# Kernel tuning notes

Hardware: AMD Instinct MI355X
Metric: run time of the kernel (lower is better)

## Reference

```python
import jax, jax.numpy as jnp
import numpy as np
from jax import lax

BATCH, FS, DIM = 32, 7, 512
E, TOPK, KD = 4, 2, 4            # experts, top-k, scan directions
N_STATE, DT_RANK = 16, 32
CAP_FACTOR, EPS, AUX_W = 1.25, 1e-6, 0.01


def _layernorm(x, g, b, eps=1e-5):
    mu = x.mean(-1, keepdims=True)
    var = ((x - mu) ** 2).mean(-1, keepdims=True)
    return (x - mu) * lax.rsqrt(var + eps) * g + b


def setup_inputs() -> dict:
    key = jax.random.key(0)
    ks = jax.random.split(key, 10)
    s = 0.02
    d = DIM
    return {
        "x": jax.random.normal(ks[0], (BATCH, FS, FS, d), jnp.float32),
        "w_gate": jax.random.normal(ks[1], (d, E)) * s,
        "b_gate": jnp.zeros((E,), jnp.float32),
        "in_proj_w": jax.random.normal(ks[2], (E, d, 2 * d)) * s,
        "in_proj_b": jnp.zeros((E, 2 * d), jnp.float32),
        "conv_w": jax.random.normal(ks[3], (E, d, 3, 3)) * s,
        "conv_b": jnp.zeros((E, d), jnp.float32),
        "x_proj_w": jax.random.normal(ks[4], (E, KD, DT_RANK + 2 * N_STATE, d)) * s,
        "dt_proj_w": jax.random.normal(ks[5], (E, KD, d, DT_RANK)) * s,
        "dt_proj_b": jax.random.normal(ks[6], (E, KD, d)) * 0.1,
        "A_log": jnp.log(jax.random.uniform(ks[7], (E, KD, d, N_STATE), minval=1.0, maxval=16.0)),
        "Ds": jnp.ones((E, KD, d), jnp.float32),
        "out_norm_g": jnp.ones((E, d), jnp.float32),
        "out_norm_b": jnp.zeros((E, d), jnp.float32),
        "norm_g": jnp.ones((E, d), jnp.float32),
        "norm_b": jnp.zeros((E, d), jnp.float32),
    }


def _ss2d_expert(x, in_w, in_b, cw, cb, xpw, dtw, dtb, A_log, Ds, og, ob, ng, nb):
    # x: [B,H,W,d]; one SS2D expert (VMamba-style, use_out_proj=False, out_norm=True)
    B, H, W, d = x.shape
    L = H * W
    xz = x @ in_w + in_b                      # [B,H,W,2d]
    xin, z = jnp.split(xz, 2, axis=-1)
    xc = jnp.transpose(xin, (0, 3, 1, 2))     # [B,d,H,W]
    xc = lax.conv_general_dilated(xc, cw[:, None, :, :], (1, 1), 'SAME',
                                  feature_group_count=d,
                                  dimension_numbers=('NCHW', 'OIHW', 'NCHW'))
    xc = jax.nn.silu(xc + cb[None, :, None, None])
    xh = xc.reshape(B, d, L)                              # row-major (h)
    xv = jnp.transpose(xc, (0, 1, 3, 2)).reshape(B, d, L)  # col-major (v)
    xs = jnp.stack([xh, xh[..., ::-1], xv, xv[..., ::-1]], axis=1)  # [B,K,d,L]

    x_dbl = jnp.einsum('bkdl,kcd->bkcl', xs, xpw)
    dt, Bm, Cm = jnp.split(x_dbl, [DT_RANK, DT_RANK + N_STATE], axis=2)
    dt = jnp.einsum('bkrl,kdr->bkdl', dt, dtw) + dtb[None, :, :, None]
    dt = jax.nn.softplus(dt)                  # [B,K,d,L]
    A = -jnp.exp(A_log)                       # [K,d,N]

    def step(h, inp):
        dt_t, B_t, C_t, x_t = inp             # [B,K,d],[B,K,N],[B,K,N],[B,K,d]
        h = h * jnp.exp(dt_t[..., None] * A) + (dt_t * x_t)[..., None] * B_t[:, :, None, :]
        y = jnp.einsum('bkdn,bkn->bkd', h, C_t)
        return h, y

    h0 = jnp.zeros((B, KD, d, N_STATE), x.dtype)
    seq = (jnp.moveaxis(dt, 3, 0), jnp.moveaxis(Bm, 3, 0),
           jnp.moveaxis(Cm, 3, 0), jnp.moveaxis(xs, 3, 0))
    _, ys = lax.scan(step, h0, seq)           # [L,B,K,d]
    ys = jnp.moveaxis(ys, 0, 3) + Ds[None, :, :, None] * xs  # [B,K,d,L]

    y = ys[:, 0] + ys[:, 1, :, ::-1]
    yv = ys[:, 2] + ys[:, 3, :, ::-1]
    y = y + jnp.transpose(yv.reshape(B, d, W, H), (0, 1, 3, 2)).reshape(B, d, L)
    y = jnp.transpose(y.reshape(B, d, H, W), (0, 2, 3, 1))   # [B,H,W,d]
    y = _layernorm(y, og, ob) * jax.nn.silu(z)
    pooled = y.mean(axis=(1, 2))              # adaptive avg pool -> [B,d]
    return _layernorm(pooled, ng, nb)


def reference(x, w_gate, b_gate, in_proj_w, in_proj_b, conv_w, conv_b, x_proj_w,
              dt_proj_w, dt_proj_b, A_log, Ds, out_norm_g, out_norm_b, norm_g, norm_b):
    B = x.shape[0]
    # gate on globally pooled features
    x_flat = x.mean(axis=(1, 2))                              # [B,dim]
    raw = jax.nn.softmax(x_flat @ w_gate + b_gate, axis=-1)   # [B,E]
    capacity = int(CAP_FACTOR * B)
    _, idx = lax.top_k(raw, TOPK)
    mask = jax.nn.one_hot(idx, E, dtype=raw.dtype).sum(axis=1)  # [B,E]
    masked = raw * mask
    denom = masked.sum(0, keepdims=True) + EPS
    gate_scores = masked / denom * capacity
    importance = raw.mean(0)
    load = mask.mean(0)
    aux_loss = AUX_W * jnp.mean((load - importance) ** 2)

    topv, topi = lax.top_k(gate_scores, TOPK)                 # [B,k]
    # dense dispatch: run every expert on the full batch (E small), then gather
    all_out = jax.vmap(_ss2d_expert, in_axes=(None,) + (0,) * 13)(
        x, in_proj_w, in_proj_b, conv_w, conv_b, x_proj_w, dt_proj_w, dt_proj_b,
        A_log, Ds, out_norm_g, out_norm_b, norm_g, norm_b)    # [E,B,dim]
    sel = all_out[topi, jnp.arange(B)[:, None]]               # [B,k,dim]
    mixed = (topv[..., None] * sel).sum(axis=1)               # [B,dim]
    return mixed, aux_loss
```

## Files before the change

### kernel.cpp

```cpp
#include <hip/hip_runtime.h>
#include <hip/hip_bf16.h>

#define B_   32
#define D_   512
#define L_   49
#define E_   4
#define KD_  4
#define NS_  16
#define RK_  32
#define JOBS_ 64

typedef short s16x8 __attribute__((ext_vector_type(8)));
typedef float f32x4v __attribute__((ext_vector_type(4)));
union U4 { uint4 u; s16x8 s; unsigned short us[8]; };

__device__ __forceinline__ float bf2f(unsigned short u){
  union{unsigned int i; float f;} v; v.i = ((unsigned int)u)<<16; return v.f;
}
__device__ __forceinline__ float2 bfp(unsigned int u){
  union{unsigned int i; float f;} a, b; a.i = u<<16; b.i = u & 0xffff0000u;
  return make_float2(a.f, b.f);
}
__device__ __forceinline__ unsigned short f2bfu(float f){
  union{float f; unsigned int i;} u; u.f = f;
  unsigned int r = u.i + 0x7fffu + ((u.i >> 16) & 1u);
  return (unsigned short)(r >> 16);
}
__device__ __forceinline__ float silu_f(float x){ return x / (1.f + expf(-x)); }

__device__ __forceinline__ float fast_exp2(float x){
  return __builtin_amdgcn_exp2f(x);
}
__device__ __forceinline__ float quad_add4(float y){
  float t1 = __uint_as_float(__builtin_amdgcn_mov_dpp(__float_as_uint(y), 0xB1, 0xF, 0xF, true));
  y += t1;
  float t2 = __uint_as_float(__builtin_amdgcn_mov_dpp(__float_as_uint(y), 0x4E, 0xF, 0xF, true));
  y += t2;
  return y;
}
__device__ __forceinline__ unsigned cvtpk_bf16(float lo, float hi){
  unsigned r; asm("v_cvt_pk_bf16_f32 %0, %1, %2" : "=v"(r) : "v"(lo), "v"(hi)); return r;
}

__device__ __forceinline__ int detect_bf(const void* x){
  unsigned short u = ((const unsigned short*)x)[threadIdx.x & 63];
  int e = (u >> 7) & 0xff;
  unsigned long long m = __ballot(e >= 96 && e < 160);
  return __popcll(m) >= 56;
}

__device__ __forceinline__ float ldf(const void* p, size_t i, int bf){
  return bf ? bf2f(((const unsigned short*)p)[i]) : ((const float*)p)[i];
}
struct f8s{ float v[8]; };
__device__ __forceinline__ f8s ldf8(const void* p, size_t i, int bf){
  f8s r;
  if (bf){
    uint4 u = *(const uint4*)((const unsigned short*)p + i);
    float2 x = bfp(u.x), y = bfp(u.y), z = bfp(u.z), w = bfp(u.w);
    r.v[0]=x.x; r.v[1]=x.y; r.v[2]=y.x; r.v[3]=y.y;
    r.v[4]=z.x; r.v[5]=z.y; r.v[6]=w.x; r.v[7]=w.y;
  } else {
    const float4* q = (const float4*)((const float*)p + i);
    float4 a = q[0], b = q[1];
    r.v[0]=a.x; r.v[1]=a.y; r.v[2]=a.z; r.v[3]=a.w;
    r.v[4]=b.x; r.v[5]=b.y; r.v[6]=b.z; r.v[7]=b.w;
  }
  return r;
}
struct f4s{ float v[4]; };
__device__ __forceinline__ f4s ldf4(const void* p, size_t i, int bf){
  f4s r;
  if (bf){
    uint2 u = *(const uint2*)((const unsigned short*)p + i);
    float2 a = bfp(u.x), b = bfp(u.y);
    r.v[0]=a.x; r.v[1]=a.y; r.v[2]=b.x; r.v[3]=b.y;
  } else {
    float4 a = *(const float4*)((const float*)p + i);
    r.v[0]=a.x; r.v[1]=a.y; r.v[2]=a.z; r.v[3]=a.w;
  }
  return r;
}
__device__ __forceinline__ U4 ldbf8(const void* p, size_t i, int bf){
  U4 r;
  if (bf){
    r.u = *(const uint4*)((const unsigned short*)p + i);
  } else {
    const float* q = (const float*)p + i;
    float4 a = *(const float4*)q, b = *(const float4*)(q+4);
    r.u.x = (unsigned)f2bfu(a.x) | ((unsigned)f2bfu(a.y) << 16);
    r.u.y = (unsigned)f2bfu(a.z) | ((unsigned)f2bfu(a.w) << 16);
    r.u.z = (unsigned)f2bfu(b.x) | ((unsigned)f2bfu(b.y) << 16);
    r.u.w = (unsigned)f2bfu(b.z) | ((unsigned)f2bfu(b.w) << 16);
  }
  return r;
}
__device__ __forceinline__ void split8(const float av[8], U4& hi, U4& lo){
  #pragma unroll
  for (int j = 0; j < 8; j++){
    union{float f; unsigned int i;} u; u.f = av[j];
    unsigned short h = (unsigned short)(u.i >> 16);
    hi.us[j] = h;
    lo.us[j] = f2bfu(av[j] - bf2f(h));
  }
}

__device__ __forceinline__ int dirmap(int k, int l){
  if (k == 0) return l;
  if (k == 1) return 48 - l;
  if (k == 2) return (l % 7) * 7 + l / 7;
  int l2 = 48 - l; return (l2 % 7) * 7 + l2 / 7;
}

__global__ __launch_bounds__(256) void k_prep(const void* __restrict__ x,
                                              const void* __restrict__ w,
                                              const void* __restrict__ wg,
                                              const void* __restrict__ bg,
                                              unsigned short* __restrict__ wt,
                                              unsigned short* __restrict__ xbf,
                                              float* __restrict__ logits){
  __shared__ unsigned short tile[64][72];
  __shared__ float red[4][4];
  __shared__ float pool[4][512];
  int bf = detect_bf(x);
  int blk = blockIdx.x;
  int t = threadIdx.x;
  if (blk < 512){
    int e = blk >> 7, cb = (blk >> 3) & 15, db = blk & 7;
    #pragma unroll
    for (int r = 0; r < 4; r++){
      int d  = r*16 + (t>>4);
      int c0 = (t&15)*4;
      size_t g = ((size_t)e*512 + db*64 + d)*1024 + cb*64 + c0;
      if (bf){
        uint2 u = *(const uint2*)((const unsigned short*)w + g);
        tile[c0+0][d] = (unsigned short)(u.x & 0xffffu);
        tile[c0+1][d] = (unsigned short)(u.x >> 16);
        tile[c0+2][d] = (unsigned short)(u.y & 0xffffu);
        tile[c0+3][d] = (unsigned short)(u.y >> 16);
      } else {
        float4 v = *(const float4*)((const float*)w + g);
        tile[c0+0][d] = f2bfu(v.x);
        tile[c0+1][d] = f2bfu(v.y);
        tile[c0+2][d] = f2bfu(v.z);
        tile[c0+3][d] = f2bfu(v.w);
      }
    }
    __syncthreads();
    #pragma unroll
    for (int r = 0; r < 2; r++){
      int o = r*256 + t;
      int c = o >> 3, d0 = (o & 7)*8;
      uint4 v = *(const uint4*)&tile[c][d0];
      *(uint4*)(wt + ((size_t)e*1024 + cb*64 + c)*512 + db*64 + d0) = v;
    }
  } else {
    int b = blk - 512;
    int wave = t >> 6, lane = t & 63;
    int d0 = lane * 8;
    float s8[8] = {};
    for (int l = wave; l < L_; l += 4){
      size_t ix = ((size_t)(b*L_ + l))*D_ + d0;
      U4 xb;
      if (bf){
        xb.u = *(const uint4*)((const unsigned short*)x + ix);
        float2 a = bfp(xb.u.x), bq = bfp(xb.u.y), c = bfp(xb.u.z), dq = bfp(xb.u.w);
        s8[0] += a.x;  s8[1] += a.y;  s8[2] += bq.x; s8[3] += bq.y;
        s8[4] += c.x;  s8[5] += c.y;  s8[6] += dq.x; s8[7] += dq.y;
      } else {
        const float* q = (const float*)x + ix;
        float4 f0 = *(const float4*)q, f1 = *(const float4*)(q+4);
        float av[8] = {f0.x,f0.y,f0.z,f0.w, f1.x,f1.y,f1.z,f1.w};
        #pragma unroll
        for (int j = 0; j < 8; j++){ xb.us[j] = f2bfu(av[j]); s8[j] += av[j]; }
      }
      *(uint4*)(xbf + ix) = xb.u;
    }
    #pragma unroll
    for (int j = 0; j < 8; j++) pool[wave][d0+j] = s8[j];
    __syncthreads();
    float p[4] = {0.f, 0.f, 0.f, 0.f};
    #pragma unroll
    for (int rep = 0; rep < 2; rep++){
      int d = t + rep*256;
      float s = pool[0][d] + pool[1][d] + pool[2][d] + pool[3][d];
      float xfd = s * (1.f/49.f);
      #pragma unroll
      for (int e = 0; e < 4; e++) p[e] = fmaf(xfd, ldf(wg, (size_t)d*E_ + e, bf), p[e]);
    }
    #pragma unroll
    for (int off = 32; off > 0; off >>= 1){
      #pragma unroll
      for (int e = 0; e < 4; e++) p[e] += __shfl_down(p[e], off, 64);
    }
    if (lane == 0){
      #pragma unroll
      for (int e = 0; e < 4; e++) red[wave][e] = p[e];
    }
    __syncthreads();
    if (t < 4)
      logits[b*4 + t] = red[0][t]+red[1][t]+red[2][t]+red[3][t] + ldf(bg, t, bf);
  }
}

__global__ __launch_bounds__(128) void k_gate2(const void* __restrict__ x,
                                               const float* __restrict__ logits,
                                               int* __restrict__ topi, float* __restrict__ topv,
                                               void* __restrict__ out){
  __shared__ float raw[B_*E_];
  __shared__ int   sel[B_];
  __shared__ float den[E_], auxp[E_];
  int bf = detect_bf(x);
  int t = threadIdx.x;
  if (t < B_){
    float l0=logits[t*4+0], l1=logits[t*4+1], l2=logits[t*4+2], l3=logits[t*4+3];
    float m = fmaxf(fmaxf(l0,l1), fmaxf(l2,l3));
    float e0=expf(l0-m), e1=expf(l1-m), e2=expf(l2-m), e3=expf(l3-m);
    float s = e0+e1+e2+e3;
    float r[4] = {e0/s, e1/s, e2/s, e3/s};
    int i1 = 0; float v1 = r[0];
    for (int e = 1; e < 4; e++) if (r[e] > v1){ v1 = r[e]; i1 = e; }
    int i2 = -1; float v2 = -1.f;
    for (int e = 0; e < 4; e++){ if (e == i1) continue; if (r[e] > v2){ v2 = r[e]; i2 = e; } }
    if (i1 < 0 || i1 > 3) i1 = 0;
    if (i2 < 0 || i2 > 3) i2 = (i1 + 1) & 3;
    sel[t] = (1<<i1) | (1<<i2);
    for (int e = 0; e < 4; e++) raw[t*4+e] = r[e];
  }
  __syncthreads();
  if (t < E_){
    float dn = 0.f, imp = 0.f, ld = 0.f;
    for (int b = 0; b < B_; b++){
      float r = raw[b*4+t];
      int bit = (sel[b] >> t) & 1;
      if (bit) dn += r;
      imp += r; ld += (float)bit;
    }
    den[t] = dn + 1e-6f;
    imp *= (1.f/B_); ld *= (1.f/B_);
    float df = ld - imp; auxp[t] = df*df;
  }
  __syncthreads();
  if (t == 0){
    float a = 0.01f * 0.25f * (auxp[0]+auxp[1]+auxp[2]+auxp[3]);
    if (bf) ((unsigned short*)out)[16384] = f2bfu(a);
    else    ((float*)out)[16384] = a;
  }
  if (t < B_){
    float gs[4];
    for (int e = 0; e < 4; e++){
      int bit = (sel[t] >> e) & 1;
      gs[e] = bit ? raw[t*4+e] * 40.f / den[e] : 0.f;
    }
    int i1 = 0; float v1 = gs[0];
    for (int e = 1; e < 4; e++) if (gs[e] > v1){ v1 = gs[e]; i1 = e; }
    int i2 = -1; float v2 = -1e30f;
    for (int e = 0; e < 4; e++){ if (e == i1) continue; if (gs[e] > v2){ v2 = gs[e]; i2 = e; } }
    if (i1 < 0 || i1 > 3) i1 = 0;
    if (i2 < 0 || i2 > 3) i2 = (i1 + 1) & 3;
    topi[t*2+0] = i1; topv[t*2+0] = v1;
    topi[t*2+1] = i2; topv[t*2+1] = v2;
  }
}

__global__ __launch_bounds__(256, 4) void k_inproj_mfma(const void* __restrict__ x,
                                                     const unsigned short* __restrict__ xbf,
                                                     const unsigned short* __restrict__ wt,
                                                     const void* __restrict__ bias,
                                                     const void* __restrict__ cw,
                                                     const void* __restrict__ cb,
                                                     const int* __restrict__ topi,
                                                     unsigned short* __restrict__ zbuf,
                                                     float* __restrict__ xc,
                                                     unsigned short* __restrict__ xchi,
                                                     unsigned short* __restrict__ xclo){
  __shared__ float xzt[49*68];
  int bf = detect_bf(x);
  int job = blockIdx.x, nt = blockIdx.y;
  int b = job >> 1;
  int e = topi[job];
  int t = threadIdx.x;
  int wave = t >> 6, lane = t & 63;
  int l16 = lane & 15, quad = lane >> 4;
  int arow = wave*16 + l16; if (arow > 48) arow = 48;
  size_t abase = ((size_t)(b*L_ + arow))*D_;
  int ct = nt*64;
  size_t bbase = ((size_t)(e*1024 + ct + l16))*D_;
  f32x4v acc[4] = {};
  for (int k0 = 0; k0 < 512; k0 += 32){
    int k = k0 + quad*8;
    U4 a; a.u = *(const uint4*)(xbf + abase + k);
    #pragma unroll
    for (int s = 0; s < 4; s++){
      U4 bb;
      bb.u = *(const uint4*)(wt + bbase + (size_t)s*16*D_ + k);
      acc[s] = __builtin_amdgcn_mfma_f32_16x16x32_bf16(a.s, bb.s, acc[s], 0, 0, 0);
    }
  }
  int rb = wave*16 + quad*4;
  if (nt >= 8){
    #pragma unroll
    for (int s = 0; s < 4; s++){
      int c = ct + s*16 + l16;
      float bv = ldf(bias, (size_t)e*1024 + c, bf);
      #pragma unroll
      for (int r = 0; r < 4; r++){
        int row = rb + r;
        if (row < L_)
          zbuf[(size_t)job*25088 + row*D_ + (c - 512)] = f2bfu(acc[s][r] + bv);
      }
    }
    return;
  }
  #pragma unroll
  for (int s = 0; s < 4; s++){
    int cl = s*16 + l16;
    float bv = ldf(bias, (size_t)e*1024 + ct + cl, bf);
    #pragma unroll
    for (int r = 0; r < 4; r++){
      int row = rb + r;
      if (row < L_) xzt[row*68 + cl] = acc[s][r] + bv;
    }
  }
  __syncthreads();
  int c = t & 63, pg = t >> 6;
  int dch = ct + c;
  float wv[9];
  #pragma unroll
  for (int j = 0; j < 9; j++) wv[j] = ldf(cw, ((size_t)(e*D_ + dch))*9 + j, bf);
  float cbv = ldf(cb, (size_t)e*D_ + dch, bf);
  for (int p = pg; p < L_; p += 4){
    int h = p / 7, w = p % 7;
    float a2 = cbv;
    #pragma unroll
    for (int dy = 0; dy < 3; dy++){
      int hh = h + dy - 1; if (hh < 0 || hh >= 7) continue;
      #pragma unroll
      for (int dx = 0; dx < 3; dx++){
        int ww = w + dx - 1; if (ww < 0 || ww >= 7) continue;
        a2 = fmaf(xzt[(hh*7+ww)*68 + c], wv[dy*3+dx], a2);
      }
    }
    float sv = a2 * (1.f/(1.f+expf(-a2)));
    size_t oix = (size_t)job*25088 + (size_t)p*D_ + dch;
    xc[oix] = sv;
    unsigned int ui = __float_as_uint(sv);
    unsigned short hh2 = (unsigned short)(ui >> 16);
    xchi[oix] = hh2;
    xclo[oix] = f2bfu(sv - bf2f(hh2));
  }
}

__global__ __launch_bounds__(256, 4) void k_xproj(const void* __restrict__ x,
                                               const void* __restrict__ xpw,
                                               const int* __restrict__ topi,
                                               const unsigned short* __restrict__ xchi,
                                               const unsigned short* __restrict__ xclo,
                                               float* __restrict__ xdbl){
  int bf = detect_bf(x);
  int kq = blockIdx.x, job = blockIdx.y;
  int k = kq & 3, q = kq >> 2;
  int t = threadIdx.x;
  int wave = t >> 6, lane = t & 63;
  int l16 = lane & 15, quad = lane >> 4;
  int e = topi[job];
  int arow = q*16 + l16; if (arow > 48) arow = 48;
  int m = dirmap(k, arow);
  const unsigned short* ahp = xchi + (size_t)job*25088 + (size_t)m*D_;
  const unsigned short* alp = xclo + (size_t)job*25088 + (size_t)m*D_;
  size_t bbase = (((size_t)(e*KD_+k))*64 + wave*16 + l16)*D_;
  f32x4v acc = {};
  for (int k0 = 0; k0 < 512; k0 += 32){
    int kk = k0 + quad*8;
    U4 Ahi, Alo;
    Ahi.u = *(const uint4*)(ahp + kk);
    Alo.u = *(const uint4*)(alp + kk);
    U4 bb = ldbf8(xpw, bbase + kk, bf);
    acc = __builtin_amdgcn_mfma_f32_16x16x32_bf16(Ahi.s, bb.s, acc, 0, 0, 0);
    acc = __builtin_amdgcn_mfma_f32_16x16x32_bf16(Alo.s, bb.s, acc, 0, 0, 0);
  }
  float* outb = xdbl + ((size_t)(job*KD_+k))*3136;
  int rb = q*16 + quad*4;
  int c = wave*16 + l16;
  #pragma unroll
  for (int r = 0; r < 4; r++){
    int row = rb + r;
    if (row < L_) outb[row*64 + c] = acc[r];
  }
}

__global__ __launch_bounds__(256, 2) void k_scan(const void* __restrict__ x,
                                              const void* __restrict__ dtw,
                                              const void* __restrict__ dtb_,
                                              const void* __restrict__ alog,
                                              const void* __restrict__ ds_,
                                              const int* __restrict__ topi,
                                              const float* __restrict__ xc,
                                              const float* __restrict__ xdbl,
                                              unsigned short* __restrict__ ybuf){
  int bf = detect_bf(x);
  int kz = blockIdx.x, job = blockIdx.y;
  int k = kz & 3, dz2 = kz >> 2;
  int t = threadIdx.x;
  int e = topi[job];
  int ek = e*KD_ + k;
  __shared__ float bc[49*32];
  __shared__ float dtl[49*260];
  const float* xdb = xdbl + ((size_t)(job*KD_+k))*3136;
  {
    const float4* src4 = (const float4*)xdb;
    for (int i = t; i < 392; i += 256){
      int row = i >> 3, c = i & 7;
      ((float4*)bc)[row*8 + c] = src4[row*16 + 8 + c];
    }
  }
  int w = t >> 6, lane = t & 63;
  {
    int l16 = lane & 15, quad4 = lane >> 4;
    U4 Bv[4];
    #pragma unroll
    for (int nt = 0; nt < 4; nt++){
      int d = dz2*256 + w*64 + nt*16 + l16;
      Bv[nt] = ldbf8(dtw, ((size_t)ek*D_ + d)*RK_ + quad4*8, bf);
    }
    f32x4v acc[4][4] = {};
    #pragma unroll
    for (int rt = 0; rt < 4; rt++){
      int arow = rt*16 + l16; if (arow > 48) arow = 48;
      const float* ap = xdb + arow*64 + quad4*8;
      float4 f0 = *(const float4*)ap, f1 = *(const float4*)(ap+4);
      float av[8] = {f0.x,f0.y,f0.z,f0.w, f1.x,f1.y,f1.z,f1.w};
      U4 Ahi, Alo;
      split8(av, Ahi, Alo);
      #pragma unroll
      for (int nt = 0; nt < 4; nt++){
        acc[rt][nt] = __builtin_amdgcn_mfma_f32_16x16x32_bf16(Ahi.s, Bv[nt].s, acc[rt][nt], 0, 0, 0);
        acc[rt][nt] = __builtin_amdgcn_mfma_f32_16x16x32_bf16(Alo.s, Bv[nt].s, acc[rt][nt], 0, 0, 0);
      }
    }
    #pragma unroll
    for (int nt = 0; nt < 4; nt++){
      int d = dz2*256 + w*64 + nt*16 + l16;
      float bias = ldf(dtb_, (size_t)ek*D_ + d, bf);
      int dloc = w*64 + nt*16 + l16;
      #pragma unroll
      for (int rt = 0; rt < 4; rt++){
        #pragma unroll
        for (int r = 0; r < 4; r++){
          int l = rt*16 + quad4*4 + r;
          if (l < L_){
            float v = acc[rt][nt][r] + bias;
            dtl[l*260 + dloc] = fmaxf(v, 0.f) + __logf(1.f + __expf(-fabsf(v)));
          }
        }
      }
    }
  }
  int q4 = (lane >> 2) * 4;
  int ng = lane & 3;
  int dgl = dz2*256 + w*64 + q4;
  float A2[4][4], Dsv[4];
  #pragma unroll
  for (int jj = 0; jj < 4; jj++){
    int dj = dgl + jj;
    f4s ar = ldf4(alog, ((size_t)ek*D_ + dj)*NS_ + ng*4, bf);
    #pragma unroll
    for (int n = 0; n < 4; n++) A2[jj][n] = -expf(ar.v[n]) * 1.44269504f;
    Dsv[jj] = ldf(ds_, (size_t)ek*D_ + dj, bf);
  }
  __syncthreads();
  float h[4][4];
  #pragma unroll
  for (int jj = 0; jj < 4; jj++)
    #pragma unroll
    for (int n = 0; n < 4; n++) h[jj][n] = 0.f;
  const float* xcb = xc + (size_t)job*25088;
  unsigned short* yb = ybuf + ((size_t)(job*KD_ + k))*25088;
  int dtbase = w*64 + q4;
  for (int c0 = 0; c0 < 49; c0 += 7){
    float4 xv[7];
    #pragma unroll
    for (int j = 0; j < 7; j++){
      int m = dirmap(k, c0 + j);
      xv[j] = *(const float4*)(xcb + (size_t)m*D_ + dgl);
    }
    #pragma unroll
    for (int j = 0; j < 7; j++){
      int l = c0 + j;
      float4 dt4 = *(const float4*)&dtl[l*260 + dtbase];
      float4 B4 = *(const float4*)&bc[l*32 + ng*4];
      float4 C4 = *(const float4*)&bc[l*32 + 16 + ng*4];
      float Ba[4] = {B4.x, B4.y, B4.z, B4.w};
      float Ca[4] = {C4.x, C4.y, C4.z, C4.w};
      float dta[4] = {dt4.x, dt4.y, dt4.z, dt4.w};
      float xa[4]  = {xv[j].x, xv[j].y, xv[j].z, xv[j].w};
      float ys[4];
      #pragma unroll
      for (int jj = 0; jj < 4; jj++){
        float dt = dta[jj], x_t = xa[jj];
        float dtx = dt * x_t;
        float y = 0.f;
        #pragma unroll
        for (int n = 0; n < 4; n++){
          float en = fast_exp2(dt * A2[jj][n]);
          h[jj][n] = fmaf(h[jj][n], en, dtx * Ba[n]);
          y = fmaf(h[jj][n], Ca[n], y);
        }
        y = quad_add4(y);
        ys[jj] = fmaf(Dsv[jj], x_t, y);
      }
      if (ng == 0){
        uint2 o;
        o.x = cvtpk_bf16(ys[0], ys[1]);
        o.y = cvtpk_bf16(ys[2], ys[3]);
        *(uint2*)(yb + (size_t)l*D_ + dgl) = o;
      }
    }
  }
}

__global__ __launch_bounds__(512) void k_final_a(const void* __restrict__ x,
                                                 const void* __restrict__ og,
                                                 const void* __restrict__ ob,
                                                 const int* __restrict__ topi,
                                                 const unsigned short* __restrict__ ybuf,
                                                 const unsigned short* __restrict__ zbuf,
                                                 float* __restrict__ partial){
  __shared__ float pool[8][512];
  int bf = detect_bf(x);
  int job = blockIdx.x, q = blockIdx.y, t = threadIdx.x;
  int wave = t >> 6, lane = t & 63;
  int e = topi[job];
  int d0 = lane*8;
  const unsigned short* yb = ybuf + (size_t)job*KD_*25088;
  const unsigned short* zb = zbuf + (size_t)job*25088;
  float g[8], o[8];
  {
    f8s gg = ldf8(og, (size_t)e*D_ + d0, bf);
    f8s oo = ldf8(ob, (size_t)e*D_ + d0, bf);
    #pragma unroll
    for (int j = 0; j < 8; j++){ g[j] = gg.v[j]; o[j] = oo.v[j]; }
  }
  float acc[8] = {};
  for (int i = wave; i <= 12; i += 8){
    int p = q + 4*i;
    if (p >= L_) break;
    float v[8] = {};
    #pragma unroll
    for (int k = 0; k < KD_; k++){
      int l = dirmap(k, p);
      U4 r; r.u = *(const uint4*)(yb + (size_t)k*25088 + (size_t)l*D_ + d0);
      #pragma unroll
      for (int j = 0; j < 8; j++) v[j] += bf2f(r.us[j]);
    }
    float s = 0.f, ss = 0.f;
    #pragma unroll
    for (int j = 0; j < 8; j++){ s += v[j]; ss += v[j]*v[j]; }
    #pragma unroll
    for (int off = 32; off > 0; off >>= 1){
      s  += __shfl_xor(s,  off, 64);
      ss += __shfl_xor(ss, off, 64);
    }
    float mu = s*(1.f/512.f);
    float var = ss*(1.f/512.f) - mu*mu;
    float rs = rsqrtf(var + 1e-5f);
    U4 zz; zz.u = *(const uint4*)(zb + (size_t)p*D_ + d0);
    #pragma unroll
    for (int j = 0; j < 8; j++){
      float zv = bf2f(zz.us[j]);
      acc[j] += ((v[j]-mu)*rs*g[j] + o[j]) * silu_f(zv);
    }
  }
  #pragma unroll
  for (int j = 0; j < 8; j++) pool[wave][d0+j] = acc[j];
  __syncthreads();
  float pd = pool[0][t]+pool[1][t]+pool[2][t]+pool[3][t]
           + pool[4][t]+pool[5][t]+pool[6][t]+pool[7][t];
  partial[((size_t)(job*4 + q))*512 + t] = pd;
}

__global__ __launch_bounds__(512) void k_finmix(const void* __restrict__ x,
                                                const void* __restrict__ ngg,
                                                const void* __restrict__ nbb,
                                                const int* __restrict__ topi,
                                                const float* __restrict__ topv,
                                                const float* __restrict__ partial,
                                                void* __restrict__ out){
  __shared__ float red[32];
  int bf = detect_bf(x);
  int b = blockIdx.x, t = threadIdx.x;
  int wave = t >> 6, lane = t & 63;
  int j0 = 2*b, j1 = 2*b + 1;
  int e0 = topi[j0], e1 = topi[j1];
  float g0 = topv[j0], g1 = topv[j1];
  const float* p0 = partial + (size_t)j0*4*512;
  const float* p1 = partial + (size_t)j1*4*512;
  float pd0 = (p0[t] + p0[512+t] + p0[1024+t] + p0[1536+t]) * (1.f/49.f);
  float pd1 = (p1[t] + p1[512+t] + p1[1024+t] + p1[1536+t]) * (1.f/49.f);
  float s0 = pd0, ss0 = pd0*pd0, s1 = pd1, ss1 = pd1*pd1;
  #pragma unroll
  for (int off = 32; off > 0; off >>= 1){
    s0  += __shfl_down(s0,  off, 64);
    ss0 += __shfl_down(ss0, off, 64);
    s1  += __shfl_down(s1,  off, 64);
    ss1 += __shfl_down(ss1, off, 64);
  }
  if (lane == 0){
    red[wave] = s0; red[8+wave] = ss0; red[16+wave] = s1; red[24+wave] = ss1;
  }
  __syncthreads();
  s0 = red[0]+red[1]+red[2]+red[3]+red[4]+red[5]+red[6]+red[7];
  ss0 = red[8]+red[9]+red[10]+red[11]+red[12]+red[13]+red[14]+red[15];
  s1 = red[16]+red[17]+red[18]+red[19]+red[20]+red[21]+red[22]+red[23];
  ss1 = red[24]+red[25]+red[26]+red[27]+red[28]+red[29]+red[30]+red[31];
  float mu0 = s0*(1.f/512.f), var0 = ss0*(1.f/512.f) - mu0*mu0;
  float rs0 = rsqrtf(var0 + 1e-5f);
  float mu1 = s1*(1.f/512.f), var1 = ss1*(1.f/512.f) - mu1*mu1;
  float rs1 = rsqrtf(var1 + 1e-5f);
  float v0 = ((pd0-mu0)*rs0*ldf(ngg, (size_t)e0*D_+t, bf) + ldf(nbb, (size_t)e0*D_+t, bf)) * g0;
  float v1 = ((pd1-mu1)*rs1*ldf(ngg, (size_t)e1*D_+t, bf) + ldf(nbb, (size_t)e1*D_+t, bf)) * g1;
  float v = v0 + v1;
  if (bf) ((unsigned short*)out)[b*D_ + t] = f2bfu(v);
  else    ((float*)out)[b*D_ + t] = v;
}

extern "C" void kernel_launch(void* const* d_in, const int* in_sizes, int n_in,
                              void* d_out, int out_size, void* d_ws, size_t ws_size,
                              hipStream_t stream){
  const void* x    = d_in[0];
  const void* wg   = d_in[1];
  const void* bg   = d_in[2];
  const void* ipw  = d_in[3];
  const void* ipb  = d_in[4];
  const void* cw   = d_in[5];
  const void* cb   = d_in[6];
  const void* xpw  = d_in[7];
  const void* dtw  = d_in[8];
  const void* dtb  = d_in[9];
  const void* alog = d_in[10];
  const void* dss  = d_in[11];
  const void* ogg  = d_in[12];
  const void* obb  = d_in[13];
  const void* ngg  = d_in[14];
  const void* nbb  = d_in[15];
  float* wsf = (float*)d_ws;
  int*   topi  = (int*)d_ws + 16;
  float* topv  = wsf + 96;
  float* logits= wsf + 256;
  float* xc    = wsf + 16640;
  float* xdbl  = wsf + 1622272;
  unsigned short* zbuf = (unsigned short*)(wsf + 2425088);
  unsigned short* ybuf   = (unsigned short*)(wsf + 3260672);
  unsigned short* wtrans = ybuf;
  unsigned short* xchi   = ybuf + 2097152;
  unsigned short* xclo   = ybuf + 3702784;
  unsigned short* xbf    = ybuf + 5308416;
  float* partial = wsf + 6471936;

  k_prep  <<<544, 256, 0, stream>>>(x, ipw, wg, bg, wtrans, xbf, logits);
  k_gate2 <<<1, 128, 0, stream>>>(x, logits, topi, topv, d_out);
  k_inproj_mfma<<<dim3(64,16), 256, 0, stream>>>(x, xbf, wtrans, ipb, cw, cb, topi, zbuf, xc, xchi, xclo);
  k_xproj <<<dim3(16,64), 256, 0, stream>>>(x, xpw, topi, xchi, xclo, xdbl);
  k_scan  <<<dim3(8,64), 256, 0, stream>>>(x, dtw, dtb, alog, dss, topi, xc, xdbl, ybuf);
  k_final_a<<<dim3(64,4), 512, 0, stream>>>(x, ogg, obb, topi, ybuf, zbuf, partial);
  k_finmix<<<32, 512, 0, stream>>>(x, ngg, nbb, topi, topv, partial, d_out);
}
```

Baseline: 219.7 us.

## Narrow in-proj column tiles and split x-proj K across waves

The in-projection kernel now computes 16-column tiles per block instead of 64, giving four times as many blocks with smaller shared memory and higher occupancy bounds. The fused depthwise conv now spreads its work over 16 position groups per block. The x-projection kernel doubles its block to 512 threads and splits the K dimension into two halves across wave groups, reducing the partial sums through shared memory. Both changes aim to expose more parallelism and latency hiding on small GEMMs, at the cost of reloading the A operand more times and an extra block sync.

```diff
diff --git a/kernel.cpp b/kernel.cpp
--- a/kernel.cpp
+++ b/kernel.cpp
@@ -263,7 +263,7 @@
   }
 }
 
-__global__ __launch_bounds__(256, 4) void k_inproj_mfma(const void* __restrict__ x,
+__global__ __launch_bounds__(256, 8) void k_inproj_mfma(const void* __restrict__ x,
                                                      const unsigned short* __restrict__ xbf,
                                                      const unsigned short* __restrict__ wt,
                                                      const void* __restrict__ bias,
@@ -274,7 +274,7 @@
                                                      float* __restrict__ xc,
                                                      unsigned short* __restrict__ xchi,
                                                      unsigned short* __restrict__ xclo){
-  __shared__ float xzt[49*68];
+  __shared__ float xzt[49*17];
   int bf = detect_bf(x);
   int job = blockIdx.x, nt = blockIdx.y;
   int b = job >> 1;
@@ -284,52 +284,40 @@
   int l16 = lane & 15, quad = lane >> 4;
   int arow = wave*16 + l16; if (arow > 48) arow = 48;
   size_t abase = ((size_t)(b*L_ + arow))*D_;
-  int ct = nt*64;
+  int ct = nt*16;
   size_t bbase = ((size_t)(e*1024 + ct + l16))*D_;
-  f32x4v acc[4] = {};
+  f32x4v acc = {};
+  #pragma unroll
   for (int k0 = 0; k0 < 512; k0 += 32){
     int k = k0 + quad*8;
-    U4 a; a.u = *(const uint4*)(xbf + abase + k);
-    #pragma unroll
-    for (int s = 0; s < 4; s++){
-      U4 bb;
-      bb.u = *(const uint4*)(wt + bbase + (size_t)s*16*D_ + k);
-      acc[s] = __builtin_amdgcn_mfma_f32_16x16x32_bf16(a.s, bb.s, acc[s], 0, 0, 0);
-    }
+    U4 a;  a.u  = *(const uint4*)(xbf + abase + k);
+    U4 bb; bb.u = *(const uint4*)(wt + bbase + k);
+    acc = __builtin_amdgcn_mfma_f32_16x16x32_bf16(a.s, bb.s, acc, 0, 0, 0);
   }
   int rb = wave*16 + quad*4;
-  if (nt >= 8){
-    #pragma unroll
-    for (int s = 0; s < 4; s++){
-      int c = ct + s*16 + l16;
-      float bv = ldf(bias, (size_t)e*1024 + c, bf);
-      #pragma unroll
-      for (int r = 0; r < 4; r++){
-        int row = rb + r;
-        if (row < L_)
-          zbuf[(size_t)job*25088 + row*D_ + (c - 512)] = f2bfu(acc[s][r] + bv);
-      }
-    }
-    return;
-  }
-  #pragma unroll
-  for (int s = 0; s < 4; s++){
-    int cl = s*16 + l16;
-    float bv = ldf(bias, (size_t)e*1024 + ct + cl, bf);
+  float bv = ldf(bias, (size_t)e*1024 + ct + l16, bf);
+  if (nt >= 32){
     #pragma unroll
     for (int r = 0; r < 4; r++){
       int row = rb + r;
-      if (row < L_) xzt[row*68 + cl] = acc[s][r] + bv;
-    }
+      if (row < L_)
+        zbuf[(size_t)job*25088 + row*D_ + (ct - 512 + l16)] = f2bfu(acc[r] + bv);
+    }
+    return;
+  }
+  #pragma unroll
+  for (int r = 0; r < 4; r++){
+    int row = rb + r;
+    if (row < L_) xzt[row*17 + l16] = acc[r] + bv;
   }
   __syncthreads();
-  int c = t & 63, pg = t >> 6;
+  int c = t & 15, pg = t >> 4;
   int dch = ct + c;
   float wv[9];
   #pragma unroll
   for (int j = 0; j < 9; j++) wv[j] = ldf(cw, ((size_t)(e*D_ + dch))*9 + j, bf);
   float cbv = ldf(cb, (size_t)e*D_ + dch, bf);
-  for (int p = pg; p < L_; p += 4){
+  for (int p = pg; p < L_; p += 16){
     int h = p / 7, w = p % 7;
     float a2 = cbv;
     #pragma unroll
@@ -338,7 +326,7 @@
       #pragma unroll
       for (int dx = 0; dx < 3; dx++){
         int ww = w + dx - 1; if (ww < 0 || ww >= 7) continue;
-        a2 = fmaf(xzt[(hh*7+ww)*68 + c], wv[dy*3+dx], a2);
+        a2 = fmaf(xzt[(hh*7+ww)*17 + c], wv[dy*3+dx], a2);
       }
     }
     float sv = a2 * (1.f/(1.f+expf(-a2)));
@@ -351,27 +339,31 @@
   }
 }
 
-__global__ __launch_bounds__(256, 4) void k_xproj(const void* __restrict__ x,
+__global__ __launch_bounds__(512, 8) void k_xproj(const void* __restrict__ x,
                                                const void* __restrict__ xpw,
                                                const int* __restrict__ topi,
                                                const unsigned short* __restrict__ xchi,
                                                const unsigned short* __restrict__ xclo,
                                                float* __restrict__ xdbl){
+  __shared__ float rsum[4*64*4];
   int bf = detect_bf(x);
   int kq = blockIdx.x, job = blockIdx.y;
   int k = kq & 3, q = kq >> 2;
   int t = threadIdx.x;
   int wave = t >> 6, lane = t & 63;
+  int wcol = wave & 3, khalf = wave >> 2;
   int l16 = lane & 15, quad = lane >> 4;
   int e = topi[job];
   int arow = q*16 + l16; if (arow > 48) arow = 48;
   int m = dirmap(k, arow);
   const unsigned short* ahp = xchi + (size_t)job*25088 + (size_t)m*D_;
   const unsigned short* alp = xclo + (size_t)job*25088 + (size_t)m*D_;
-  size_t bbase = (((size_t)(e*KD_+k))*64 + wave*16 + l16)*D_;
+  size_t bbase = (((size_t)(e*KD_+k))*64 + wcol*16 + l16)*D_;
+  int kbase = khalf*256;
   f32x4v acc = {};
-  for (int k0 = 0; k0 < 512; k0 += 32){
-    int kk = k0 + quad*8;
+  #pragma unroll
+  for (int k0 = 0; k0 < 256; k0 += 32){
+    int kk = kbase + k0 + quad*8;
     U4 Ahi, Alo;
     Ahi.u = *(const uint4*)(ahp + kk);
     Alo.u = *(const uint4*)(alp + kk);
@@ -379,13 +371,20 @@
     acc = __builtin_amdgcn_mfma_f32_16x16x32_bf16(Ahi.s, bb.s, acc, 0, 0, 0);
     acc = __builtin_amdgcn_mfma_f32_16x16x32_bf16(Alo.s, bb.s, acc, 0, 0, 0);
   }
-  float* outb = xdbl + ((size_t)(job*KD_+k))*3136;
-  int rb = q*16 + quad*4;
-  int c = wave*16 + l16;
-  #pragma unroll
-  for (int r = 0; r < 4; r++){
-    int row = rb + r;
-    if (row < L_) outb[row*64 + c] = acc[r];
+  if (khalf == 1){
+    #pragma unroll
+    for (int r = 0; r < 4; r++) rsum[(wcol*64 + lane)*4 + r] = acc[r];
+  }
+  __syncthreads();
+  if (khalf == 0){
+    float* outb = xdbl + ((size_t)(job*KD_+k))*3136;
+    int rb = q*16 + quad*4;
+    int c = wcol*16 + l16;
+    #pragma unroll
+    for (int r = 0; r < 4; r++){
+      int row = rb + r;
+      if (row < L_) outb[row*64 + c] = acc[r] + rsum[(wcol*64 + lane)*4 + r];
+    }
   }
 }
 
@@ -659,8 +658,8 @@
 
   k_prep  <<<544, 256, 0, stream>>>(x, ipw, wg, bg, wtrans, xbf, logits);
   k_gate2 <<<1, 128, 0, stream>>>(x, logits, topi, topv, d_out);
-  k_inproj_mfma<<<dim3(64,16), 256, 0, stream>>>(x, xbf, wtrans, ipb, cw, cb, topi, zbuf, xc, xchi, xclo);
-  k_xproj <<<dim3(16,64), 256, 0, stream>>>(x, xpw, topi, xchi, xclo, xdbl);
+  k_inproj_mfma<<<dim3(64,64), 256, 0, stream>>>(x, xbf, wtrans, ipb, cw, cb, topi, zbuf, xc, xchi, xclo);
+  k_xproj <<<dim3(16,64), 512, 0, stream>>>(x, xpw, topi, xchi, xclo, xdbl);
   k_scan  <<<dim3(8,64), 256, 0, stream>>>(x, dtw, dtb, alog, dss, topi, xc, xdbl, ybuf);
   k_final_a<<<dim3(64,4), 512, 0, stream>>>(x, ogg, obb, topi, ybuf, zbuf, partial);
   k_finmix<<<32, 512, 0, stream>>>(x, ngg, nbb, topi, topv, partial, d_out);
```

Result: slower. 234.9 us (+6.9%).
